# Performance work log

Hardware: AMD Instinct MI355X
Metric: run time of the kernel (lower is better)

Reference implementation:

```python
import jax, jax.numpy as jnp
import numpy as np

B = 8192
EMBED = 4  # self-attention embed dim


def setup_inputs() -> dict:
    key = jax.random.key(0)
    ks = jax.random.split(key, 20)
    f32 = jnp.float32
    return {
        "inputs": jax.random.normal(ks[0], (B, 8), dtype=f32),
        # MLP chain params (stored as [in, out]; y = x @ W + b)
        "W_fm": jax.random.normal(ks[1], (8, 16), dtype=f32) * 0.1,
        "b_fm": jnp.zeros((16,), dtype=f32),
        "W_c1": jax.random.normal(ks[2], (16, 16), dtype=f32) * 0.1,
        "b_c1": jnp.zeros((16,), dtype=f32),
        "W_p1": jax.random.normal(ks[3], (16, 12), dtype=f32) * 0.1,
        "b_p1": jnp.zeros((12,), dtype=f32),
        "W_c2": jax.random.normal(ks[4], (12, 8), dtype=f32) * 0.1,
        "b_c2": jnp.zeros((8,), dtype=f32),
        "W_p2": jax.random.normal(ks[5], (8, 4), dtype=f32) * 0.1,
        "b_p2": jnp.zeros((4,), dtype=f32),
        "W_c3": jax.random.normal(ks[6], (4, 4), dtype=f32) * 0.1,
        "b_c3": jnp.zeros((4,), dtype=f32),
        # self-attention params
        "rot": jax.random.normal(ks[7], (EMBED, EMBED), dtype=f32),
        "ent": jax.random.normal(ks[8], (EMBED, EMBED), dtype=f32),
        # ConvFilter: 2x2 conv kernel flattened (cross-correlation over 2x2 patch)
        "conv_w": jax.random.normal(ks[9], (4,), dtype=f32) * 0.5,
        "conv_b": jnp.zeros((1,), dtype=f32),
        # head: Linear(1,1)
        "head_w": jax.random.normal(ks[10], (1, 1), dtype=f32),
        "head_b": jnp.zeros((1,), dtype=f32),
    }


def reference(inputs, W_fm, b_fm, W_c1, b_c1, W_p1, b_p1, W_c2, b_c2,
              W_p2, b_p2, W_c3, b_c3, rot, ent, conv_w, conv_b,
              head_w, head_b):
    threshold = 0.0
    shift = 0.0
    # MLP chain: Linear + Tanh blocks
    x = jnp.tanh(inputs @ W_fm + b_fm)   # [B,16]
    x = jnp.tanh(x @ W_c1 + b_c1)        # [B,16]
    x = jnp.tanh(x @ W_p1 + b_p1)        # [B,12]
    x = jnp.tanh(x @ W_c2 + b_c2)        # [B,8]
    x = jnp.tanh(x @ W_p2 + b_p2)        # [B,4]
    x = jnp.tanh(x @ W_c3 + b_c3)        # [B,4]
    # self-attention over the batch axis (as in the original torch.mm)
    q = x @ rot                           # [B,4]
    k = x @ ent                           # [B,4]
    scores = jax.nn.softmax((q @ k.T) / jnp.sqrt(jnp.float32(EMBED)), axis=-1)  # [B,B]
    x = scores @ x                        # [B,4]
    # batched 2x2 conv filter: each sample's 4-vector reshaped to 2x2, one
    # valid conv output -> sum(w * patch) + b; mean of single elem is itself
    filtered = jax.nn.sigmoid(x @ conv_w + conv_b - threshold)[:, None]  # [B,1]
    logits = filtered @ head_w + head_b   # [B,1]
    return jax.nn.sigmoid(logits + shift)
```

## Files before the change

kernel.cpp:

```cpp
#include <hip/hip_runtime.h>
#include <math.h>

#define BATCH 8192
#define BLK 256
#define NSPLIT 32
#define CHUNK (BATCH / NSPLIT)


template <int IN, int OUT>
__device__ __forceinline__ void layer_tanh(const float* a, float* out,
                                           const float* __restrict__ W,
                                           const float* __restrict__ bias) {
  float acc[OUT];
#pragma unroll
  for (int o = 0; o < OUT; o++) acc[o] = bias[o];
#pragma unroll
  for (int i = 0; i < IN; i++) {
    float ai = a[i];
#pragma unroll
    for (int o = 0; o < OUT; o++) acc[o] = fmaf(ai, W[i * OUT + o], acc[o]);
  }
#pragma unroll
  for (int o = 0; o < OUT; o++) out[o] = tanhf(acc[o]);
}

__global__ __launch_bounds__(BLK) void mlp_kernel(
    const float* __restrict__ in,
    const float* __restrict__ W_fm, const float* __restrict__ b_fm,
    const float* __restrict__ W_c1, const float* __restrict__ b_c1,
    const float* __restrict__ W_p1, const float* __restrict__ b_p1,
    const float* __restrict__ W_c2, const float* __restrict__ b_c2,
    const float* __restrict__ W_p2, const float* __restrict__ b_p2,
    const float* __restrict__ W_c3, const float* __restrict__ b_c3,
    const float* __restrict__ rot, const float* __restrict__ ent,
    float4* __restrict__ qv, float4* __restrict__ kvx) {
  __shared__ float w[812];
  const int t = threadIdx.x;
  auto cp = [&](const float* src, int off, int n) {
    for (int i = t; i < n; i += BLK) w[off + i] = src[i];
  };
  cp(W_fm, 0, 128);  cp(b_fm, 128, 16);
  cp(W_c1, 144, 256); cp(b_c1, 400, 16);
  cp(W_p1, 416, 192); cp(b_p1, 608, 12);
  cp(W_c2, 620, 96);  cp(b_c2, 716, 8);
  cp(W_p2, 724, 32);  cp(b_p2, 756, 4);
  cp(W_c3, 760, 16);  cp(b_c3, 776, 4);
  cp(rot, 780, 16);   cp(ent, 796, 16);
  __syncthreads();

  const int r = blockIdx.x * BLK + t;
  const float4* in4 = (const float4*)in;
  float4 i0 = in4[r * 2 + 0];
  float4 i1 = in4[r * 2 + 1];
  float a[16], b[16];
  a[0] = i0.x; a[1] = i0.y; a[2] = i0.z; a[3] = i0.w;
  a[4] = i1.x; a[5] = i1.y; a[6] = i1.z; a[7] = i1.w;

  layer_tanh<8, 16>(a, b, w + 0, w + 128);
  layer_tanh<16, 16>(b, a, w + 144, w + 400);
  layer_tanh<16, 12>(a, b, w + 416, w + 608);
  layer_tanh<12, 8>(b, a, w + 620, w + 716);
  layer_tanh<8, 4>(a, b, w + 724, w + 756);
  layer_tanh<4, 4>(b, a, w + 760, w + 776);
  float q[4], k[4];
#pragma unroll
  for (int d = 0; d < 4; d++) {
    q[d] = a[0] * w[780 + 0 * 4 + d] + a[1] * w[780 + 1 * 4 + d] +
           a[2] * w[780 + 2 * 4 + d] + a[3] * w[780 + 3 * 4 + d];
    k[d] = a[0] * w[796 + 0 * 4 + d] + a[1] * w[796 + 1 * 4 + d] +
           a[2] * w[796 + 2 * 4 + d] + a[3] * w[796 + 3 * 4 + d];
  }
  qv[r] = make_float4(q[0] * 0.5f, q[1] * 0.5f, q[2] * 0.5f, q[3] * 0.5f);
  kvx[2 * r + 0] = make_float4(k[0], k[1], k[2], k[3]);
  kvx[2 * r + 1] = make_float4(a[0], a[1], a[2], a[3]);
}

__device__ __forceinline__ float dot4(float4 a, float4 b) {
  return fmaf(a.x, b.x, fmaf(a.y, b.y, fmaf(a.z, b.z, a.w * b.w)));
}

__global__ __launch_bounds__(BLK) void attn_partial(
    const float4* __restrict__ kvx, const float4* __restrict__ qv,
    float* __restrict__ l_arr, float4* __restrict__ o_arr) {
  const int t = threadIdx.x;
  const int qi = blockIdx.x * BLK + t;
  const int c0 = blockIdx.y * CHUNK;
  const float4 q = qv[qi];

  float l0 = 0.f, l1 = 0.f;
  float4 o0 = make_float4(0.f, 0.f, 0.f, 0.f);
  float4 o1 = make_float4(0.f, 0.f, 0.f, 0.f);
#pragma unroll 4
  for (int j = 0; j < CHUNK; j += 2) {
    const float4 ka = kvx[(c0 + j) * 2 + 0];
    const float4 va = kvx[(c0 + j) * 2 + 1];
    const float4 kb = kvx[(c0 + j) * 2 + 2];
    const float4 vb = kvx[(c0 + j) * 2 + 3];
    float s0 = dot4(q, ka);
    float s1 = dot4(q, kb);
    float p0 = __expf(s0);
    float p1 = __expf(s1);
    l0 += p0;
    l1 += p1;
    o0.x = fmaf(p0, va.x, o0.x); o0.y = fmaf(p0, va.y, o0.y);
    o0.z = fmaf(p0, va.z, o0.z); o0.w = fmaf(p0, va.w, o0.w);
    o1.x = fmaf(p1, vb.x, o1.x); o1.y = fmaf(p1, vb.y, o1.y);
    o1.z = fmaf(p1, vb.z, o1.z); o1.w = fmaf(p1, vb.w, o1.w);
  }
  const int idx = blockIdx.y * BATCH + qi;
  l_arr[idx] = l0 + l1;
  o_arr[idx] = make_float4(o0.x + o1.x, o0.y + o1.y, o0.z + o1.z, o0.w + o1.w);
}

__global__ __launch_bounds__(BLK) void combine_kernel(
    const float* __restrict__ l_arr, const float4* __restrict__ o_arr,
    const float* __restrict__ conv_w, const float* __restrict__ conv_b,
    const float* __restrict__ head_w, const float* __restrict__ head_b,
    float* __restrict__ out) {
  const int qi = blockIdx.x * BLK + threadIdx.x;
  float l = 0.f;
  float4 o = make_float4(0.f, 0.f, 0.f, 0.f);
#pragma unroll
  for (int s = 0; s < NSPLIT; s++) {
    l += l_arr[s * BATCH + qi];
    float4 os = o_arr[s * BATCH + qi];
    o.x += os.x; o.y += os.y; o.z += os.z; o.w += os.w;
  }
  const float inv = 1.0f / l;
  float z = o.x * inv * conv_w[0] + o.y * inv * conv_w[1] +
            o.z * inv * conv_w[2] + o.w * inv * conv_w[3] + conv_b[0];
  float filtered = 1.0f / (1.0f + __expf(-z));
  float logit = fmaf(filtered, head_w[0], head_b[0]);
  out[qi] = 1.0f / (1.0f + __expf(-logit));
}

extern "C" void kernel_launch(void* const* d_in, const int* in_sizes, int n_in,
                              void* d_out, int out_size, void* d_ws,
                              size_t ws_size, hipStream_t stream) {
  const float* in   = (const float*)d_in[0];
  const float* W_fm = (const float*)d_in[1];
  const float* b_fm = (const float*)d_in[2];
  const float* W_c1 = (const float*)d_in[3];
  const float* b_c1 = (const float*)d_in[4];
  const float* W_p1 = (const float*)d_in[5];
  const float* b_p1 = (const float*)d_in[6];
  const float* W_c2 = (const float*)d_in[7];
  const float* b_c2 = (const float*)d_in[8];
  const float* W_p2 = (const float*)d_in[9];
  const float* b_p2 = (const float*)d_in[10];
  const float* W_c3 = (const float*)d_in[11];
  const float* b_c3 = (const float*)d_in[12];
  const float* rot  = (const float*)d_in[13];
  const float* ent  = (const float*)d_in[14];
  const float* conv_w = (const float*)d_in[15];
  const float* conv_b = (const float*)d_in[16];
  const float* head_w = (const float*)d_in[17];
  const float* head_b = (const float*)d_in[18];
  float* out = (float*)d_out;

  char* ws = (char*)d_ws;
  float4* qv  = (float4*)(ws + 0);
  float4* kvx = (float4*)(ws + (128 << 10));
  float*  l_arr = (float*)(ws + (384 << 10));
  float4* o_arr = (float4*)(ws + (384 << 10) + NSPLIT * BATCH * 4);

  mlp_kernel<<<BATCH / BLK, BLK, 0, stream>>>(
      in, W_fm, b_fm, W_c1, b_c1, W_p1, b_p1, W_c2, b_c2, W_p2, b_p2, W_c3,
      b_c3, rot, ent, qv, kvx);

  dim3 grid(BATCH / BLK, NSPLIT);
  attn_partial<<<grid, BLK, 0, stream>>>(kvx, qv, l_arr, o_arr);

  combine_kernel<<<BATCH / BLK, BLK, 0, stream>>>(
      l_arr, o_arr, conv_w, conv_b, head_w, head_b, out);
}
```

Before: 130.7 us.

## Fuse combine into attention via last-block tickets, shrink MLP blocks, use exp2

The separate combine kernel is removed. Each attention block now increments an atomic ticket per query chunk, and the last split block to finish reduces the partial sums and applies the conv and sigmoid head. This saves one kernel launch and its dependency gap. The MLP kernel now uses 64-thread blocks so more CUs are busy, and it zeroes the tickets. The query is pre-scaled by log2(e) so the inner loop can call exp2f, and the unroll factor rises to 8. The cost is atomic and fence overhead, plus a dependence on tickets being reset before the attention launch.

```diff
diff --git a/kernel.cpp b/kernel.cpp
--- a/kernel.cpp
+++ b/kernel.cpp
@@ -3,8 +3,10 @@
 
 #define BATCH 8192
 #define BLK 256
+#define BLKM 64
 #define NSPLIT 32
 #define CHUNK (BATCH / NSPLIT)
+#define NQCHUNK (BATCH / BLK)
 
 
 template <int IN, int OUT>
@@ -24,7 +26,7 @@
   for (int o = 0; o < OUT; o++) out[o] = tanhf(acc[o]);
 }
 
-__global__ __launch_bounds__(BLK) void mlp_kernel(
+__global__ __launch_bounds__(BLKM) void mlp_kernel(
     const float* __restrict__ in,
     const float* __restrict__ W_fm, const float* __restrict__ b_fm,
     const float* __restrict__ W_c1, const float* __restrict__ b_c1,
@@ -33,11 +35,13 @@
     const float* __restrict__ W_p2, const float* __restrict__ b_p2,
     const float* __restrict__ W_c3, const float* __restrict__ b_c3,
     const float* __restrict__ rot, const float* __restrict__ ent,
-    float4* __restrict__ qv, float4* __restrict__ kvx) {
+    float4* __restrict__ qv, float4* __restrict__ kvx,
+    unsigned* __restrict__ tickets) {
   __shared__ float w[812];
   const int t = threadIdx.x;
+  if (blockIdx.x == 0 && t < NQCHUNK) tickets[t] = 0u;
   auto cp = [&](const float* src, int off, int n) {
-    for (int i = t; i < n; i += BLK) w[off + i] = src[i];
+    for (int i = t; i < n; i += BLKM) w[off + i] = src[i];
   };
   cp(W_fm, 0, 128);  cp(b_fm, 128, 16);
   cp(W_c1, 144, 256); cp(b_c1, 400, 16);
@@ -48,7 +52,7 @@
   cp(rot, 780, 16);   cp(ent, 796, 16);
   __syncthreads();
 
-  const int r = blockIdx.x * BLK + t;
+  const int r = blockIdx.x * BLKM + t;
   const float4* in4 = (const float4*)in;
   float4 i0 = in4[r * 2 + 0];
   float4 i1 = in4[r * 2 + 1];
@@ -70,7 +74,8 @@
     k[d] = a[0] * w[796 + 0 * 4 + d] + a[1] * w[796 + 1 * 4 + d] +
            a[2] * w[796 + 2 * 4 + d] + a[3] * w[796 + 3 * 4 + d];
   }
-  qv[r] = make_float4(q[0] * 0.5f, q[1] * 0.5f, q[2] * 0.5f, q[3] * 0.5f);
+  const float SC = 0.5f * 1.44269504088896340736f;
+  qv[r] = make_float4(q[0] * SC, q[1] * SC, q[2] * SC, q[3] * SC);
   kvx[2 * r + 0] = make_float4(k[0], k[1], k[2], k[3]);
   kvx[2 * r + 1] = make_float4(a[0], a[1], a[2], a[3]);
 }
@@ -79,9 +84,13 @@
   return fmaf(a.x, b.x, fmaf(a.y, b.y, fmaf(a.z, b.z, a.w * b.w)));
 }
 
-__global__ __launch_bounds__(BLK) void attn_partial(
+__global__ __launch_bounds__(BLK) void attn_kernel(
     const float4* __restrict__ kvx, const float4* __restrict__ qv,
-    float* __restrict__ l_arr, float4* __restrict__ o_arr) {
+    float* __restrict__ l_arr, float4* __restrict__ o_arr,
+    unsigned* __restrict__ tickets,
+    const float* __restrict__ conv_w, const float* __restrict__ conv_b,
+    const float* __restrict__ head_w, const float* __restrict__ head_b,
+    float* __restrict__ out) {
   const int t = threadIdx.x;
   const int qi = blockIdx.x * BLK + t;
   const int c0 = blockIdx.y * CHUNK;
@@ -90,7 +99,7 @@
   float l0 = 0.f, l1 = 0.f;
   float4 o0 = make_float4(0.f, 0.f, 0.f, 0.f);
   float4 o1 = make_float4(0.f, 0.f, 0.f, 0.f);
-#pragma unroll 4
+#pragma unroll 8
   for (int j = 0; j < CHUNK; j += 2) {
     const float4 ka = kvx[(c0 + j) * 2 + 0];
     const float4 va = kvx[(c0 + j) * 2 + 1];
@@ -98,8 +107,8 @@
     const float4 vb = kvx[(c0 + j) * 2 + 3];
     float s0 = dot4(q, ka);
     float s1 = dot4(q, kb);
-    float p0 = __expf(s0);
-    float p1 = __expf(s1);
+    float p0 = exp2f(s0);
+    float p1 = exp2f(s1);
     l0 += p0;
     l1 += p1;
     o0.x = fmaf(p0, va.x, o0.x); o0.y = fmaf(p0, va.y, o0.y);
@@ -110,28 +119,28 @@
   const int idx = blockIdx.y * BATCH + qi;
   l_arr[idx] = l0 + l1;
   o_arr[idx] = make_float4(o0.x + o1.x, o0.y + o1.y, o0.z + o1.z, o0.w + o1.w);
-}
 
-__global__ __launch_bounds__(BLK) void combine_kernel(
-    const float* __restrict__ l_arr, const float4* __restrict__ o_arr,
-    const float* __restrict__ conv_w, const float* __restrict__ conv_b,
-    const float* __restrict__ head_w, const float* __restrict__ head_b,
-    float* __restrict__ out) {
-  const int qi = blockIdx.x * BLK + threadIdx.x;
-  float l = 0.f;
-  float4 o = make_float4(0.f, 0.f, 0.f, 0.f);
+  __shared__ unsigned tick;
+  __threadfence();
+  if (t == 0) tick = atomicAdd(&tickets[blockIdx.x], 1u);
+  __syncthreads();
+  if (tick == NSPLIT - 1) {
+    __threadfence();
+    float l = 0.f;
+    float4 o = make_float4(0.f, 0.f, 0.f, 0.f);
 #pragma unroll
-  for (int s = 0; s < NSPLIT; s++) {
-    l += l_arr[s * BATCH + qi];
-    float4 os = o_arr[s * BATCH + qi];
-    o.x += os.x; o.y += os.y; o.z += os.z; o.w += os.w;
+    for (int s = 0; s < NSPLIT; s++) {
+      l += l_arr[s * BATCH + qi];
+      float4 os = o_arr[s * BATCH + qi];
+      o.x += os.x; o.y += os.y; o.z += os.z; o.w += os.w;
+    }
+    const float inv = 1.0f / l;
+    float z = o.x * inv * conv_w[0] + o.y * inv * conv_w[1] +
+              o.z * inv * conv_w[2] + o.w * inv * conv_w[3] + conv_b[0];
+    float filtered = 1.0f / (1.0f + __expf(-z));
+    float logit = fmaf(filtered, head_w[0], head_b[0]);
+    out[qi] = 1.0f / (1.0f + __expf(-logit));
   }
-  const float inv = 1.0f / l;
-  float z = o.x * inv * conv_w[0] + o.y * inv * conv_w[1] +
-            o.z * inv * conv_w[2] + o.w * inv * conv_w[3] + conv_b[0];
-  float filtered = 1.0f / (1.0f + __expf(-z));
-  float logit = fmaf(filtered, head_w[0], head_b[0]);
-  out[qi] = 1.0f / (1.0f + __expf(-logit));
 }
 
 extern "C" void kernel_launch(void* const* d_in, const int* in_sizes, int n_in,
@@ -159,18 +168,17 @@
   float* out = (float*)d_out;
 
   char* ws = (char*)d_ws;
-  float4* qv  = (float4*)(ws + 0);
-  float4* kvx = (float4*)(ws + (128 << 10));
-  float*  l_arr = (float*)(ws + (384 << 10));
-  float4* o_arr = (float4*)(ws + (384 << 10) + NSPLIT * BATCH * 4);
+  float4*   qv      = (float4*)(ws + 0);
+  float4*   kvx     = (float4*)(ws + (128 << 10));
+  float*    l_arr   = (float*)(ws + (384 << 10));
+  float4*   o_arr   = (float4*)(ws + (384 << 10) + NSPLIT * BATCH * 4);
+  unsigned* tickets = (unsigned*)(ws + (384 << 10) + NSPLIT * BATCH * 20);
 
-  mlp_kernel<<<BATCH / BLK, BLK, 0, stream>>>(
+  mlp_kernel<<<BATCH / BLKM, BLKM, 0, stream>>>(
       in, W_fm, b_fm, W_c1, b_c1, W_p1, b_p1, W_c2, b_c2, W_p2, b_p2, W_c3,
-      b_c3, rot, ent, qv, kvx);
+      b_c3, rot, ent, qv, kvx, tickets);
 
-  dim3 grid(BATCH / BLK, NSPLIT);
-  attn_partial<<<grid, BLK, 0, stream>>>(kvx, qv, l_arr, o_arr);
-
-  combine_kernel<<<BATCH / BLK, BLK, 0, stream>>>(
-      l_arr, o_arr, conv_w, conv_b, head_w, head_b, out);
+  dim3 grid(NQCHUNK, NSPLIT);
+  attn_kernel<<<grid, BLK, 0, stream>>>(kvx, qv, l_arr, o_arr, tickets,
+                                        conv_w, conv_b, head_w, head_b, out);
 }
```

Result: slower. 209.9 us (+60.6%).

## Fuse attention and combine by splitting each query's keys across half-wave lanes

Applied to the files above, without the earlier changes.

The separate split-K attention pass and the combine kernel are replaced by one attention kernel. In it, 32 lanes share one query, each lane strides over a slice of keys, and the partial sums are reduced with wave shuffles before the sigmoid head is applied. The query is pre-scaled by log2(e) so the inner loop can call exp2f. The MLP kernel block size also drops to 64. This removes the partial-result round trip through global memory and one launch, but each lane now loads distinct keys instead of broadcast keys, which greatly increases L1/L2 load traffic.

```diff
diff --git a/kernel.cpp b/kernel.cpp
--- a/kernel.cpp
+++ b/kernel.cpp
@@ -2,9 +2,8 @@
 #include <math.h>
 
 #define BATCH 8192
-#define BLK 256
-#define NSPLIT 32
-#define CHUNK (BATCH / NSPLIT)
+#define BLKM 64
+#define BLKA 256
 
 
 template <int IN, int OUT>
@@ -24,7 +23,7 @@
   for (int o = 0; o < OUT; o++) out[o] = tanhf(acc[o]);
 }
 
-__global__ __launch_bounds__(BLK) void mlp_kernel(
+__global__ __launch_bounds__(BLKM) void mlp_kernel(
     const float* __restrict__ in,
     const float* __restrict__ W_fm, const float* __restrict__ b_fm,
     const float* __restrict__ W_c1, const float* __restrict__ b_c1,
@@ -37,7 +36,7 @@
   __shared__ float w[812];
   const int t = threadIdx.x;
   auto cp = [&](const float* src, int off, int n) {
-    for (int i = t; i < n; i += BLK) w[off + i] = src[i];
+    for (int i = t; i < n; i += BLKM) w[off + i] = src[i];
   };
   cp(W_fm, 0, 128);  cp(b_fm, 128, 16);
   cp(W_c1, 144, 256); cp(b_c1, 400, 16);
@@ -48,7 +47,7 @@
   cp(rot, 780, 16);   cp(ent, 796, 16);
   __syncthreads();
 
-  const int r = blockIdx.x * BLK + t;
+  const int r = blockIdx.x * BLKM + t;
   const float4* in4 = (const float4*)in;
   float4 i0 = in4[r * 2 + 0];
   float4 i1 = in4[r * 2 + 1];
@@ -70,7 +69,8 @@
     k[d] = a[0] * w[796 + 0 * 4 + d] + a[1] * w[796 + 1 * 4 + d] +
            a[2] * w[796 + 2 * 4 + d] + a[3] * w[796 + 3 * 4 + d];
   }
-  qv[r] = make_float4(q[0] * 0.5f, q[1] * 0.5f, q[2] * 0.5f, q[3] * 0.5f);
+  const float SC = 0.5f * 1.44269504088896340736f;
+  qv[r] = make_float4(q[0] * SC, q[1] * SC, q[2] * SC, q[3] * SC);
   kvx[2 * r + 0] = make_float4(k[0], k[1], k[2], k[3]);
   kvx[2 * r + 1] = make_float4(a[0], a[1], a[2], a[3]);
 }
@@ -79,59 +79,52 @@
   return fmaf(a.x, b.x, fmaf(a.y, b.y, fmaf(a.z, b.z, a.w * b.w)));
 }
 
-__global__ __launch_bounds__(BLK) void attn_partial(
+__global__ __launch_bounds__(BLKA) void attn_kernel(
     const float4* __restrict__ kvx, const float4* __restrict__ qv,
-    float* __restrict__ l_arr, float4* __restrict__ o_arr) {
-  const int t = threadIdx.x;
-  const int qi = blockIdx.x * BLK + t;
-  const int c0 = blockIdx.y * CHUNK;
-  const float4 q = qv[qi];
-
-  float l0 = 0.f, l1 = 0.f;
-  float4 o0 = make_float4(0.f, 0.f, 0.f, 0.f);
-  float4 o1 = make_float4(0.f, 0.f, 0.f, 0.f);
-#pragma unroll 4
-  for (int j = 0; j < CHUNK; j += 2) {
-    const float4 ka = kvx[(c0 + j) * 2 + 0];
-    const float4 va = kvx[(c0 + j) * 2 + 1];
-    const float4 kb = kvx[(c0 + j) * 2 + 2];
-    const float4 vb = kvx[(c0 + j) * 2 + 3];
-    float s0 = dot4(q, ka);
-    float s1 = dot4(q, kb);
-    float p0 = __expf(s0);
-    float p1 = __expf(s1);
-    l0 += p0;
-    l1 += p1;
-    o0.x = fmaf(p0, va.x, o0.x); o0.y = fmaf(p0, va.y, o0.y);
-    o0.z = fmaf(p0, va.z, o0.z); o0.w = fmaf(p0, va.w, o0.w);
-    o1.x = fmaf(p1, vb.x, o1.x); o1.y = fmaf(p1, vb.y, o1.y);
-    o1.z = fmaf(p1, vb.z, o1.z); o1.w = fmaf(p1, vb.w, o1.w);
-  }
-  const int idx = blockIdx.y * BATCH + qi;
-  l_arr[idx] = l0 + l1;
-  o_arr[idx] = make_float4(o0.x + o1.x, o0.y + o1.y, o0.z + o1.z, o0.w + o1.w);
-}
-
-__global__ __launch_bounds__(BLK) void combine_kernel(
-    const float* __restrict__ l_arr, const float4* __restrict__ o_arr,
     const float* __restrict__ conv_w, const float* __restrict__ conv_b,
     const float* __restrict__ head_w, const float* __restrict__ head_b,
     float* __restrict__ out) {
-  const int qi = blockIdx.x * BLK + threadIdx.x;
+  const int t = threadIdx.x;
+  const int wave = t >> 6;
+  const int lane = t & 63;
+  const int qsub = lane >> 5;
+  const int slice = lane & 31;
+  const int qi = blockIdx.x * 8 + wave * 2 + qsub;
+  const float4 q = qv[qi];
+
   float l = 0.f;
   float4 o = make_float4(0.f, 0.f, 0.f, 0.f);
+#pragma unroll 4
+  for (int j = 0; j < BATCH / 32; j++) {
+    const int key = j * 32 + slice;
+    const float4 k4 = kvx[2 * key + 0];
+    const float4 v4 = kvx[2 * key + 1];
+    float s = dot4(q, k4);
+    float p = exp2f(s);
+    l += p;
+    o.x = fmaf(p, v4.x, o.x);
+    o.y = fmaf(p, v4.y, o.y);
+    o.z = fmaf(p, v4.z, o.z);
+    o.w = fmaf(p, v4.w, o.w);
+  }
+
 #pragma unroll
-  for (int s = 0; s < NSPLIT; s++) {
-    l += l_arr[s * BATCH + qi];
-    float4 os = o_arr[s * BATCH + qi];
-    o.x += os.x; o.y += os.y; o.z += os.z; o.w += os.w;
+  for (int m = 16; m >= 1; m >>= 1) {
+    l += __shfl_xor(l, m, 64);
+    o.x += __shfl_xor(o.x, m, 64);
+    o.y += __shfl_xor(o.y, m, 64);
+    o.z += __shfl_xor(o.z, m, 64);
+    o.w += __shfl_xor(o.w, m, 64);
   }
-  const float inv = 1.0f / l;
-  float z = o.x * inv * conv_w[0] + o.y * inv * conv_w[1] +
-            o.z * inv * conv_w[2] + o.w * inv * conv_w[3] + conv_b[0];
-  float filtered = 1.0f / (1.0f + __expf(-z));
-  float logit = fmaf(filtered, head_w[0], head_b[0]);
-  out[qi] = 1.0f / (1.0f + __expf(-logit));
+
+  if (slice == 0) {
+    const float inv = 1.0f / l;
+    float z = o.x * inv * conv_w[0] + o.y * inv * conv_w[1] +
+              o.z * inv * conv_w[2] + o.w * inv * conv_w[3] + conv_b[0];
+    float filtered = 1.0f / (1.0f + __expf(-z));
+    float logit = fmaf(filtered, head_w[0], head_b[0]);
+    out[qi] = 1.0f / (1.0f + __expf(-logit));
+  }
 }
 
 extern "C" void kernel_launch(void* const* d_in, const int* in_sizes, int n_in,
@@ -161,16 +154,11 @@
   char* ws = (char*)d_ws;
   float4* qv  = (float4*)(ws + 0);
   float4* kvx = (float4*)(ws + (128 << 10));
-  float*  l_arr = (float*)(ws + (384 << 10));
-  float4* o_arr = (float4*)(ws + (384 << 10) + NSPLIT * BATCH * 4);
 
-  mlp_kernel<<<BATCH / BLK, BLK, 0, stream>>>(
+  mlp_kernel<<<BATCH / BLKM, BLKM, 0, stream>>>(
       in, W_fm, b_fm, W_c1, b_c1, W_p1, b_p1, W_c2, b_c2, W_p2, b_p2, W_c3,
       b_c3, rot, ent, qv, kvx);
 
-  dim3 grid(BATCH / BLK, NSPLIT);
-  attn_partial<<<grid, BLK, 0, stream>>>(kvx, qv, l_arr, o_arr);
-
-  combine_kernel<<<BATCH / BLK, BLK, 0, stream>>>(
-      l_arr, o_arr, conv_w, conv_b, head_w, head_b, out);
+  attn_kernel<<<BATCH / 8, BLKA, 0, stream>>>(kvx, qv, conv_w, conv_b,
+                                              head_w, head_b, out);
 }
```

Result: slower. 158.4 us (+21.2%).
